# Performance work log

Measured on AMD Instinct MI355X. Metric: run time of the kernel, lower is better.

## Reference

```python
import jax, jax.numpy as jnp
import numpy as np

V, E, H, LM, LC = 50257, 512, 1024, 128, 256


def gru_cell(x, h, Wih, Whh, bih, bhh):
    # PyTorch nn.GRU cell, gate order (r, z, n)
    gi = x @ Wih.T + bih
    gh = h @ Whh.T + bhh
    i_r, i_z, i_n = jnp.split(gi, 3, -1)
    h_r, h_z, h_n = jnp.split(gh, 3, -1)
    r = jax.nn.sigmoid(i_r + h_r)
    z = jax.nn.sigmoid(i_z + h_z)
    n = jnp.tanh(i_n + r * h_n)
    return (1.0 - z) * n + z * h


def setup_inputs() -> dict:
    key = jax.random.key(0)
    ks = jax.random.split(key, 18)
    f = lambda k, sh: jax.random.normal(k, sh, jnp.float32) * 0.02
    return {
        "motion": jax.random.randint(ks[0], (1, LM), 0, V),
        "target_output": jax.random.randint(ks[1], (1, LC), 0, V),
        "enc_emb": f(ks[2], (V, E)),
        "enc_Wih": f(ks[3], (3 * H, E)),
        "enc_Whh": f(ks[4], (3 * H, H)),
        "enc_bih": f(ks[5], (3 * H,)),
        "enc_bhh": f(ks[6], (3 * H,)),
        "dec_emb": f(ks[7], (V, H)),
        "dec_Wih": f(ks[8], (3 * H, H)),
        "dec_Whh": f(ks[9], (3 * H, H)),
        "dec_bih": f(ks[10], (3 * H,)),
        "dec_bhh": f(ks[11], (3 * H,)),
        "attn_W": f(ks[12], (LM, 2 * H)),
        "attn_b": f(ks[13], (LM,)),
        "comb_W": f(ks[14], (H, 2 * H)),
        "comb_b": f(ks[15], (H,)),
        "out_W": f(ks[16], (V, H)),
        "out_b": f(ks[17], (V,)),
    }


def reference(motion, target_output, enc_emb, enc_Wih, enc_Whh, enc_bih, enc_bhh,
              dec_emb, dec_Wih, dec_Whh, dec_bih, dec_bhh,
              attn_W, attn_b, comb_W, comb_b, out_W, out_b):
    # ----- encode: per-step GRU over motion tokens (batch is hard-coded 1) -----
    toks = motion[0]  # [LM]

    def enc_step(h, t):
        h2 = gru_cell(enc_emb[t], h, enc_Wih, enc_Whh, enc_bih, enc_bhh)
        return h2, h2

    h0 = jnp.zeros((H,), jnp.float32)
    enc_h, enc_outs = jax.lax.scan(enc_step, h0, toks)  # enc_outs: [LM, H]

    # ----- decode with teacher forcing -----
    # original: decoder_input = SOS at idx 0, then target[idx-1] set at end of
    # step idx => step idx+1 consumes target[idx-1]; step 1 consumes target[-1].
    tgt = target_output[0]  # [LC]
    dec_in = jnp.concatenate([jnp.zeros((1,), tgt.dtype), tgt[-1:], tgt[:-2]])  # [LC]

    def dec_step(h, t):
        emb = dec_emb[t]  # [H] (dropout is identity at inference)
        attn_w = jax.nn.softmax(jnp.concatenate([emb, h]) @ attn_W.T + attn_b)  # [LM]
        ctx = attn_w @ enc_outs  # [H]
        x = jnp.concatenate([emb, ctx]) @ comb_W.T + comb_b  # [H] (no relu in source)
        h2 = gru_cell(x, h, dec_Wih, dec_Whh, dec_bih, dec_bhh)
        logp = jax.nn.log_softmax(h2 @ out_W.T + out_b)  # [V]
        return h2, logp

    _, logps = jax.lax.scan(dec_step, enc_h, dec_in)  # [LC, V]
    return logps[None]  # [1, LC, V] (permute(1,0,2) with batch=1)
```

## Files before the change

### kernel.cpp

```cpp
#include <hip/hip_runtime.h>

#define V_ 50257
#define E_ 512
#define H_ 1024
#define LM_ 128
#define LC_ 256
#define NBLK 256
#define ROWS 12

typedef __attribute__((ext_vector_type(8))) short short8;
typedef __attribute__((ext_vector_type(4))) float f32x4;
typedef unsigned long long u64;

__device__ __forceinline__ unsigned short f2bf(float x) {
  union { float f; unsigned u; } v; v.f = x;
  unsigned r = v.u + 0x7fffu + ((v.u >> 16) & 1u);
  return (unsigned short)(r >> 16);
}
__device__ __forceinline__ float bflo(unsigned u) { union { unsigned u; float f; } v; v.u = u << 16; return v.f; }
__device__ __forceinline__ float bfhi(unsigned u) { union { unsigned u; float f; } v; v.u = u & 0xffff0000u; return v.f; }

__device__ __forceinline__ int grow4(int s, int i0) {
  return (s < 4) ? (i0 + s) : (s < 8) ? (1024 + i0 + (s - 4)) : (2048 + i0 + (s - 8));
}

__device__ __forceinline__ void st_u32(unsigned* p, unsigned v) {
  __hip_atomic_store(p, v, __ATOMIC_RELAXED, __HIP_MEMORY_SCOPE_AGENT);
}
__device__ __forceinline__ void st_u64(u64* p, u64 v) {
  __hip_atomic_store(p, v, __ATOMIC_RELAXED, __HIP_MEMORY_SCOPE_AGENT);
}
__device__ __forceinline__ u64 ld_u64(const u64* p) {
  return __hip_atomic_load(p, __ATOMIC_RELAXED, __HIP_MEMORY_SCOPE_AGENT);
}
__device__ __forceinline__ unsigned ld_u32(const unsigned* p) {
  return __hip_atomic_load(p, __ATOMIC_RELAXED, __HIP_MEMORY_SCOPE_AGENT);
}
__device__ __forceinline__ float ld_f32(const float* p) {
  return __hip_atomic_load(p, __ATOMIC_RELAXED, __HIP_MEMORY_SCOPE_AGENT);
}
__device__ __forceinline__ void atom_add_f32(float* p, float v) {
  (void)__hip_atomic_fetch_add(p, v, __ATOMIC_RELAXED, __HIP_MEMORY_SCOPE_AGENT);
}

__device__ __forceinline__ void wait_flags4(const unsigned* flags, unsigned need, int tid) {
  if (tid < 64) {
    for (;;) {
      unsigned f0 = ld_u32(&flags[tid * 16]);
      unsigned f1 = ld_u32(&flags[(tid + 64) * 16]);
      unsigned f2 = ld_u32(&flags[(tid + 128) * 16]);
      unsigned f3 = ld_u32(&flags[(tid + 192) * 16]);
      unsigned mn = min(min(f0, f1), min(f2, f3));
      if (__all((int)(mn >= need))) break;
      __builtin_amdgcn_s_sleep(2);
    }
  }
  __syncthreads();
}

__global__ void gather_enc(const int* __restrict__ motion, const float* __restrict__ emb,
                           float* __restrict__ dst) {
  int t = blockIdx.x;
  int tok = motion[t];
  const float4* s = (const float4*)(emb + (size_t)tok * E_);
  float4* d = (float4*)(dst + (size_t)t * E_);
  d[threadIdx.x] = s[threadIdx.x];
}

__global__ void gather_dec(const int* __restrict__ tgt, const float* __restrict__ emb,
                           float* __restrict__ dst) {
  int t = blockIdx.x;
  int tok = (t == 0) ? 0 : (t == 1 ? tgt[LC_ - 1] : tgt[t - 2]);
  const float4* s = (const float4*)(emb + (size_t)tok * H_);
  float4* d = (float4*)(dst + (size_t)t * H_);
  d[threadIdx.x] = s[threadIdx.x];
}

__global__ __launch_bounds__(256) void gemm_f32(const float* __restrict__ A, int lda,
                                                const float* __restrict__ B, int ldb,
                                                const float* __restrict__ bias,
                                                float* __restrict__ C, int ldc, int K) {
  __shared__ float As[16][68];
  __shared__ float Bs[16][68];
  const int bm = blockIdx.y * 64, bn = blockIdx.x * 64;
  const int tid = threadIdx.x;
  const int tx = tid & 15, ty = tid >> 4;
  const int lm = tid & 63, lk = (tid >> 6) * 4;
  float acc[4][4] = {};
  for (int k0 = 0; k0 < K; k0 += 16) {
    float4 av = *(const float4*)&A[(size_t)(bm + lm) * lda + k0 + lk];
    float4 bv = *(const float4*)&B[(size_t)(bn + lm) * ldb + k0 + lk];
    As[lk + 0][lm] = av.x; As[lk + 1][lm] = av.y; As[lk + 2][lm] = av.z; As[lk + 3][lm] = av.w;
    Bs[lk + 0][lm] = bv.x; Bs[lk + 1][lm] = bv.y; Bs[lk + 2][lm] = bv.z; Bs[lk + 3][lm] = bv.w;
    __syncthreads();
#pragma unroll
    for (int kk = 0; kk < 16; ++kk) {
      float4 a4 = *(const float4*)&As[kk][ty * 4];
      float4 b4 = *(const float4*)&Bs[kk][tx * 4];
      acc[0][0] += a4.x * b4.x; acc[0][1] += a4.x * b4.y; acc[0][2] += a4.x * b4.z; acc[0][3] += a4.x * b4.w;
      acc[1][0] += a4.y * b4.x; acc[1][1] += a4.y * b4.y; acc[1][2] += a4.y * b4.z; acc[1][3] += a4.y * b4.w;
      acc[2][0] += a4.z * b4.x; acc[2][1] += a4.z * b4.y; acc[2][2] += a4.z * b4.z; acc[2][3] += a4.z * b4.w;
      acc[3][0] += a4.w * b4.x; acc[3][1] += a4.w * b4.y; acc[3][2] += a4.w * b4.z; acc[3][3] += a4.w * b4.w;
    }
    __syncthreads();
  }
#pragma unroll
  for (int i = 0; i < 4; ++i) {
#pragma unroll
    for (int j = 0; j < 4; ++j) {
      int gm = bm + ty * 4 + i, gn = bn + tx * 4 + j;
      float bv = bias ? bias[gn] : 0.f;
      C[(size_t)gm * ldc + gn] = acc[i][j] + bv;
    }
  }
}

__global__ __launch_bounds__(256) void enc_rnn(const float* __restrict__ Whh,
                                               const float* __restrict__ bhh,
                                               const float* __restrict__ gi,
                                               u64* __restrict__ hx,
                                               unsigned* __restrict__ eflags,
                                               float* __restrict__ outs) {
  __shared__ unsigned short Whl[ROWS][1024];
  __shared__ unsigned h_sh[512];
  __shared__ float h_own[4];
  __shared__ float bh[ROWS];
  __shared__ float ghl[ROWS];
  const int b = blockIdx.x, tid = threadIdx.x;
  const int w = tid >> 6, l = tid & 63;
  const int i0 = b * 4;
  for (int idx = tid; idx < ROWS * 1024; idx += 256) {
    int s = idx >> 10, c = idx & 1023;
    Whl[s][c] = f2bf(Whh[(size_t)grow4(s, i0) * H_ + c]);
  }
  if (tid < ROWS) bh[tid] = bhh[grow4(tid, i0)];
  if (tid < 4) h_own[tid] = 0.f;
  __syncthreads();

  for (int t = 0; t < LM_; ++t) {
    if (t == 0) {
      h_sh[2 * tid] = 0u; h_sh[2 * tid + 1] = 0u;
    } else {
      wait_flags4(eflags, (unsigned)t, tid);
      u64 v = ld_u64(&hx[(t & 1) * 256 + tid]);
      h_sh[2 * tid] = (unsigned)v;
      h_sh[2 * tid + 1] = (unsigned)(v >> 32);
    }
    __syncthreads();

    for (int s = w; s < ROWS; s += 4) {
      float acc = 0.f;
#pragma unroll
      for (int e = 0; e < 8; ++e) {
        unsigned u = *(const unsigned*)&Whl[s][2 * (e * 64 + l)];
        unsigned hv = h_sh[e * 64 + l];
        acc += bflo(u) * bflo(hv) + bfhi(u) * bfhi(hv);
      }
#pragma unroll
      for (int off = 32; off; off >>= 1) acc += __shfl_xor(acc, off);
      if (l == 0) ghl[s] = acc;
    }
    __syncthreads();
    float hpv = 0.f;
    if (tid < 4) {
      int i = tid, ig = i0 + i;
      const float* git = gi + (size_t)t * 3072;
      float gr = git[ig], gz = git[1024 + ig], gn = git[2048 + ig];
      float hr = ghl[i] + bh[i], hz = ghl[4 + i] + bh[4 + i], hn = ghl[8 + i] + bh[8 + i];
      float r = 1.f / (1.f + expf(-(gr + hr)));
      float z = 1.f / (1.f + expf(-(gz + hz)));
      float n = tanhf(gn + r * hn);
      hpv = (1.f - z) * n + z * h_own[i];
      h_own[i] = hpv;
      outs[(size_t)t * H_ + ig] = hpv;
      float v0 = __shfl(hpv, 0), v1 = __shfl(hpv, 1);
      float v2 = __shfl(hpv, 2), v3 = __shfl(hpv, 3);
      if (tid == 0) {
        u64 pk = (u64)((unsigned)f2bf(v0) | ((unsigned)f2bf(v1) << 16))
               | ((u64)((unsigned)f2bf(v2) | ((unsigned)f2bf(v3) << 16)) << 32);
        st_u64(&hx[((t + 1) & 1) * 256 + b], pk);
      }
    }
    __syncthreads();
    if (tid == 0) st_u32(&eflags[b * 16], (unsigned)(t + 1));
  }
}

__global__ __launch_bounds__(256) void dec_rnn(const float* __restrict__ Whh,
                                               const float* __restrict__ bhh,
                                               const float* __restrict__ attn_W,
                                               const float* __restrict__ G,
                                               const float* __restrict__ P1,
                                               const float* __restrict__ aE,
                                               const float* __restrict__ hfin,
                                               float* __restrict__ a_acc,
                                               u64* __restrict__ hx,
                                               unsigned* __restrict__ dflags,
                                               unsigned short* __restrict__ Hs) {
  __shared__ unsigned short Whl[ROWS][1024];
  __shared__ unsigned Ac[2 * 128];
  __shared__ float Gl[ROWS][128];
  __shared__ unsigned h_sh[512];
  __shared__ float a_f[128];
  __shared__ float h_own[4];
  __shared__ float bh[ROWS];
  __shared__ float ghl[ROWS];
  __shared__ float giS[ROWS];
  const int b = blockIdx.x, tid = threadIdx.x;
  const int w = tid >> 6, l = tid & 63;
  const int i0 = b * 4;
  for (int idx = tid; idx < ROWS * 1024; idx += 256) {
    int s = idx >> 10, c = idx & 1023;
    Whl[s][c] = f2bf(Whh[(size_t)grow4(s, i0) * H_ + c]);
  }
  if (tid < 256) {
    int u = tid >> 7, j = tid & 127;
    float2 wv = *(const float2*)&attn_W[(size_t)j * 2048 + 1024 + i0 + 2 * u];
    Ac[tid] = (unsigned)f2bf(wv.x) | ((unsigned)f2bf(wv.y) << 16);
  }
  for (int idx = tid; idx < ROWS * 128; idx += 256) {
    int s = idx >> 7, c = idx & 127;
    Gl[s][c] = G[(size_t)grow4(s, i0) * 128 + c];
  }
  if (tid < ROWS) bh[tid] = bhh[grow4(tid, i0)];
  if (tid < 4) h_own[tid] = hfin[i0 + tid];
  __syncthreads();

  {
    float h0 = h_own[0], h1 = h_own[1], h2 = h_own[2], h3 = h_own[3];
    if (tid < 128) {
      unsigned w0 = Ac[tid], w1 = Ac[128 + tid];
      float a0 = bflo(w0) * h0 + bfhi(w0) * h1 + bflo(w1) * h2 + bfhi(w1) * h3;
      atom_add_f32(&a_acc[(b & 3) * 128 + tid], a0);
    }
    __syncthreads();
    if (tid == 0) st_u32(&dflags[b * 16], 1u);
  }

  for (int t = 0; t < LC_; ++t) {
    wait_flags4(dflags, (unsigned)(t + 1), tid);
    if (t == 0) {
      float4 hv = ((const float4*)hfin)[tid];
      h_sh[2 * tid] = (unsigned)f2bf(hv.x) | ((unsigned)f2bf(hv.y) << 16);
      h_sh[2 * tid + 1] = (unsigned)f2bf(hv.z) | ((unsigned)f2bf(hv.w) << 16);
    } else {
      u64 v = ld_u64(&hx[(t & 1) * 256 + tid]);
      h_sh[2 * tid] = (unsigned)v;
      h_sh[2 * tid + 1] = (unsigned)(v >> 32);
    }
    if (tid < 128) {
      const float* ab = a_acc + (size_t)t * 512;
      a_f[tid] = ld_f32(&ab[tid]) + ld_f32(&ab[128 + tid]) + ld_f32(&ab[256 + tid])
               + ld_f32(&ab[384 + tid]) + aE[(size_t)t * LM_ + tid];
    }
    __syncthreads();

    float ax = a_f[2 * l], ay = a_f[2 * l + 1];
    float mx = fmaxf(ax, ay);
#pragma unroll
    for (int off = 32; off; off >>= 1) mx = fmaxf(mx, __shfl_xor(mx, off));
    float pe0 = expf(ax - mx), pe1 = expf(ay - mx);
    float zs = pe0 + pe1;
#pragma unroll
    for (int off = 32; off; off >>= 1) zs += __shfl_xor(zs, off);
    float w0 = pe0 / zs, w1 = pe1 / zs;
    for (int s = w; s < ROWS; s += 4) {
      float2 g2 = *(const float2*)&Gl[s][2 * l];
      float acc = g2.x * w0 + g2.y * w1;
#pragma unroll
      for (int off = 32; off; off >>= 1) acc += __shfl_xor(acc, off);
      if (l == 0) giS[s] = acc + P1[(size_t)t * 3072 + grow4(s, i0)];
    }
    for (int s = w; s < ROWS; s += 4) {
      float acc = 0.f;
#pragma unroll
      for (int e = 0; e < 8; ++e) {
        unsigned u = *(const unsigned*)&Whl[s][2 * (e * 64 + l)];
        unsigned hv = h_sh[e * 64 + l];
        acc += bflo(u) * bflo(hv) + bfhi(u) * bfhi(hv);
      }
#pragma unroll
      for (int off = 32; off; off >>= 1) acc += __shfl_xor(acc, off);
      if (l == 0) ghl[s] = acc;
    }
    __syncthreads();

    float hpv = 0.f;
    if (tid < 4) {
      int i = tid, ig = i0 + i;
      float hr = ghl[i] + bh[i], hz = ghl[4 + i] + bh[4 + i], hn = ghl[8 + i] + bh[8 + i];
      float r = 1.f / (1.f + expf(-(giS[i] + hr)));
      float z = 1.f / (1.f + expf(-(giS[4 + i] + hz)));
      float n = tanhf(giS[8 + i] + r * hn);
      hpv = (1.f - z) * n + z * h_own[i];
      h_own[i] = hpv;
      Hs[(size_t)t * H_ + ig] = f2bf(hpv);
      if (t < LC_ - 1) {
        float v0 = __shfl(hpv, 0), v1 = __shfl(hpv, 1);
        float v2 = __shfl(hpv, 2), v3 = __shfl(hpv, 3);
        if (tid == 0) {
          u64 pk = (u64)((unsigned)f2bf(v0) | ((unsigned)f2bf(v1) << 16))
                 | ((u64)((unsigned)f2bf(v2) | ((unsigned)f2bf(v3) << 16)) << 32);
          st_u64(&hx[((t + 1) & 1) * 256 + b], pk);
        }
      }
    }
    __syncthreads();
    if (t < LC_ - 1) {
      float h0 = h_own[0], h1 = h_own[1], h2 = h_own[2], h3 = h_own[3];
      if (tid < 128) {
        unsigned w0p = Ac[tid], w1p = Ac[128 + tid];
        float a0 = bflo(w0p) * h0 + bfhi(w0p) * h1 + bflo(w1p) * h2 + bfhi(w1p) * h3;
        atom_add_f32(&a_acc[(size_t)(t + 1) * 512 + (b & 3) * 128 + tid], a0);
      }
    }
    __syncthreads();
    if (tid == 0) st_u32(&dflags[b * 16], (unsigned)(t + 2));
  }
}

__global__ __launch_bounds__(256) void out_gemm(const unsigned short* __restrict__ A,
                                                const float* __restrict__ Wf,
                                                const float* __restrict__ bias,
                                                float* __restrict__ C, int N, int K) {
  __shared__ unsigned short As[256][40];
  __shared__ unsigned short Bs[64][40];
  const int bn = blockIdx.x * 64;
  const int tid = threadIdx.x, w = tid >> 6, l = tid & 63;
  f32x4 acc[4][4];
#pragma unroll
  for (int mf = 0; mf < 4; ++mf)
#pragma unroll
    for (int nf = 0; nf < 4; ++nf) acc[mf][nf] = (f32x4){0.f, 0.f, 0.f, 0.f};

  for (int k0 = 0; k0 < K; k0 += 32) {
    const unsigned short* src = A + (size_t)tid * K + k0;
#pragma unroll
    for (int kc = 0; kc < 4; ++kc) {
      short8 v = *(const short8*)(src + kc * 8);
      *(short8*)&As[tid][kc * 8] = v;
    }
#pragma unroll
    for (int c = 0; c < 2; ++c) {
      int idx = tid + c * 256;
      int n = idx >> 3, kc = idx & 7;
      int gn = bn + n;
      float4 v = {0.f, 0.f, 0.f, 0.f};
      if (gn < N) v = *(const float4*)&Wf[(size_t)gn * K + k0 + kc * 4];
      uint2 p;
      p.x = (unsigned)f2bf(v.x) | ((unsigned)f2bf(v.y) << 16);
      p.y = (unsigned)f2bf(v.z) | ((unsigned)f2bf(v.w) << 16);
      *(uint2*)&Bs[n][kc * 4] = p;
    }
    __syncthreads();
    const int k8 = (l >> 4) * 8;
    short8 af4[4], bf4[4];
#pragma unroll
    for (int mf = 0; mf < 4; ++mf) af4[mf] = *(const short8*)&As[w * 64 + mf * 16 + (l & 15)][k8];
#pragma unroll
    for (int nf = 0; nf < 4; ++nf) bf4[nf] = *(const short8*)&Bs[nf * 16 + (l & 15)][k8];
#pragma unroll
    for (int mf = 0; mf < 4; ++mf)
#pragma unroll
      for (int nf = 0; nf < 4; ++nf)
        acc[mf][nf] = __builtin_amdgcn_mfma_f32_16x16x32_bf16(af4[mf], bf4[nf], acc[mf][nf], 0, 0, 0);
    __syncthreads();
  }
#pragma unroll
  for (int mf = 0; mf < 4; ++mf) {
#pragma unroll
    for (int nf = 0; nf < 4; ++nf) {
      int n = bn + nf * 16 + (l & 15);
      if (n < N) {
        float bv = bias[n];
#pragma unroll
        for (int i = 0; i < 4; ++i) {
          int m = w * 64 + mf * 16 + (l >> 4) * 4 + i;
          C[(size_t)m * N + n] = acc[mf][nf][i] + bv;
        }
      }
    }
  }
}

__global__ __launch_bounds__(256) void lsm_stats(const float* __restrict__ C, float* __restrict__ stats, int N) {
  const int r = blockIdx.x, tid = threadIdx.x, w = tid >> 6, l = tid & 63;
  __shared__ float red[4];
  const float* row = C + (size_t)r * N;
  float m = -3.4e38f;
  for (int i = tid; i < N; i += 256) m = fmaxf(m, row[i]);
#pragma unroll
  for (int off = 32; off; off >>= 1) m = fmaxf(m, __shfl_xor(m, off));
  if (l == 0) red[w] = m;
  __syncthreads();
  m = fmaxf(fmaxf(red[0], red[1]), fmaxf(red[2], red[3]));
  __syncthreads();
  float s = 0.f;
  for (int i = tid; i < N; i += 256) s += expf(row[i] - m);
#pragma unroll
  for (int off = 32; off; off >>= 1) s += __shfl_xor(s, off);
  if (l == 0) red[w] = s;
  __syncthreads();
  if (tid == 0) {
    stats[r] = m;
    stats[256 + r] = logf(red[0] + red[1] + red[2] + red[3]);
  }
}

__global__ __launch_bounds__(256) void lsm_apply(float* __restrict__ C, const float* __restrict__ stats, int N) {
  int r = blockIdx.y;
  int ci = blockIdx.x * 256 + threadIdx.x;
  if (ci < N) {
    size_t idx = (size_t)r * N + ci;
    C[idx] = C[idx] - stats[r] - stats[256 + r];
  }
}

extern "C" void kernel_launch(void* const* d_in, const int* in_sizes, int n_in,
                              void* d_out, int out_size, void* d_ws, size_t ws_size,
                              hipStream_t stream) {
  (void)in_sizes; (void)n_in; (void)out_size; (void)ws_size;
  const int* motion = (const int*)d_in[0];
  const int* tgt = (const int*)d_in[1];
  const float* enc_emb = (const float*)d_in[2];
  const float* enc_Wih = (const float*)d_in[3];
  const float* enc_Whh = (const float*)d_in[4];
  const float* enc_bih = (const float*)d_in[5];
  const float* enc_bhh = (const float*)d_in[6];
  const float* dec_emb = (const float*)d_in[7];
  const float* dec_Wih = (const float*)d_in[8];
  const float* dec_Whh = (const float*)d_in[9];
  const float* dec_bih = (const float*)d_in[10];
  const float* dec_bhh = (const float*)d_in[11];
  const float* attn_W = (const float*)d_in[12];
  const float* attn_b = (const float*)d_in[13];
  const float* comb_W = (const float*)d_in[14];
  const float* comb_b = (const float*)d_in[15];
  const float* out_W = (const float*)d_in[16];
  const float* out_b = (const float*)d_in[17];
  float* out = (float*)d_out;

  float* wsf = (float*)d_ws;
  size_t o = 0;
  auto F = [&](size_t n) { float* p = wsf + o; o += (n + 3) & ~(size_t)3; return p; };
  float* enc_gi = F(128 * 3072);
  float* enc_outs = F(128 * 1024);
  float* embA = F(128 * 512);
  float* demb = F(256 * 1024);
  float* aE = F(256 * 128);
  float* xE = F(256 * 1024);
  float* P1 = F(256 * 3072);
  float* M2T = F(128 * 1024);
  float* Gm = F(3072 * 128);
  u64* hx = (u64*)F(1024);
  unsigned* eflags = (unsigned*)F(4096);
  unsigned* dflags = (unsigned*)F(4096);
  float* a_acc = F(LC_ * 4 * 128);
  float* stats = F(512);
  unsigned short* Hs = (unsigned short*)F(256 * 1024 / 2);

  hipMemsetAsync(eflags, 0, (4096 + 4096 + LC_ * 4 * 128) * sizeof(float), stream);

  gather_enc<<<128, 128, 0, stream>>>(motion, enc_emb, embA);
  gemm_f32<<<dim3(48, 2), 256, 0, stream>>>(embA, 512, enc_Wih, 512, enc_bih, enc_gi, 3072, 512);
  gather_dec<<<256, 256, 0, stream>>>(tgt, dec_emb, demb);
  gemm_f32<<<dim3(2, 4), 256, 0, stream>>>(demb, 1024, attn_W, 2048, attn_b, aE, 128, 1024);
  gemm_f32<<<dim3(16, 4), 256, 0, stream>>>(demb, 1024, comb_W, 2048, comb_b, xE, 1024, 1024);
  gemm_f32<<<dim3(48, 4), 256, 0, stream>>>(xE, 1024, dec_Wih, 1024, dec_bih, P1, 3072, 1024);

  enc_rnn<<<NBLK, 256, 0, stream>>>(enc_Whh, enc_bhh, enc_gi, hx, eflags, enc_outs);

  gemm_f32<<<dim3(16, 2), 256, 0, stream>>>(enc_outs, 1024, comb_W + 1024, 2048, nullptr, M2T, 1024, 1024);
  gemm_f32<<<dim3(2, 48), 256, 0, stream>>>(dec_Wih, 1024, M2T, 1024, nullptr, Gm, 128, 1024);

  dec_rnn<<<NBLK, 256, 0, stream>>>(dec_Whh, dec_bhh, attn_W, Gm, P1, aE,
                                    enc_outs + (size_t)(LM_ - 1) * H_, a_acc, hx, dflags, Hs);

  out_gemm<<<786, 256, 0, stream>>>(Hs, out_W, out_b, out, V_, 1024);
  lsm_stats<<<256, 256, 0, stream>>>(out, stats, V_);
  lsm_apply<<<dim3(197, 256), 256, 0, stream>>>(out, stats, V_);
}
```

Measured before the change: 2.701 ms.

## Tag hidden-state packets with step counters and overlap recurrent matvec with flag wait

Result: slower. 2.845 ms (+5.3%).

```diff
diff --git a/kernel.cpp b/kernel.cpp
--- a/kernel.cpp
+++ b/kernel.cpp
@@ -43,21 +43,6 @@
   (void)__hip_atomic_fetch_add(p, v, __ATOMIC_RELAXED, __HIP_MEMORY_SCOPE_AGENT);
 }
 
-__device__ __forceinline__ void wait_flags4(const unsigned* flags, unsigned need, int tid) {
-  if (tid < 64) {
-    for (;;) {
-      unsigned f0 = ld_u32(&flags[tid * 16]);
-      unsigned f1 = ld_u32(&flags[(tid + 64) * 16]);
-      unsigned f2 = ld_u32(&flags[(tid + 128) * 16]);
-      unsigned f3 = ld_u32(&flags[(tid + 192) * 16]);
-      unsigned mn = min(min(f0, f1), min(f2, f3));
-      if (__all((int)(mn >= need))) break;
-      __builtin_amdgcn_s_sleep(2);
-    }
-  }
-  __syncthreads();
-}
-
 __global__ void gather_enc(const int* __restrict__ motion, const float* __restrict__ emb,
                            float* __restrict__ dst) {
   int t = blockIdx.x;
@@ -74,6 +59,16 @@
   const float4* s = (const float4*)(emb + (size_t)tok * H_);
   float4* d = (float4*)(dst + (size_t)t * H_);
   d[threadIdx.x] = s[threadIdx.x];
+}
+
+__global__ void cvt_bf16(const float* __restrict__ src, u64* __restrict__ dst, int n) {
+  int i = (blockIdx.x * 256 + threadIdx.x) * 4;
+  if (i < n) {
+    float4 v = *(const float4*)&src[i];
+    u64 pk = (u64)((unsigned)f2bf(v.x) | ((unsigned)f2bf(v.y) << 16))
+           | ((u64)((unsigned)f2bf(v.z) | ((unsigned)f2bf(v.w) << 16)) << 32);
+    dst[i >> 2] = pk;
+  }
 }
 
 __global__ __launch_bounds__(256) void gemm_f32(const float* __restrict__ A, int lda,
@@ -118,8 +113,7 @@
 __global__ __launch_bounds__(256) void enc_rnn(const float* __restrict__ Whh,
                                                const float* __restrict__ bhh,
                                                const float* __restrict__ gi,
-                                               u64* __restrict__ hx,
-                                               unsigned* __restrict__ eflags,
+                                               u64* __restrict__ epk,
                                                float* __restrict__ outs) {
   __shared__ unsigned short Whl[ROWS][1024];
   __shared__ unsigned h_sh[512];
@@ -141,10 +135,15 @@
     if (t == 0) {
       h_sh[2 * tid] = 0u; h_sh[2 * tid + 1] = 0u;
     } else {
-      wait_flags4(eflags, (unsigned)t, tid);
-      u64 v = ld_u64(&hx[(t & 1) * 256 + tid]);
-      h_sh[2 * tid] = (unsigned)v;
-      h_sh[2 * tid + 1] = (unsigned)(v >> 32);
+      const u64* pb = epk + (size_t)(t & 1) * 512 + 2 * tid;
+      const unsigned g = (unsigned)t;
+      u64 q0, q1;
+      for (;;) {
+        q0 = ld_u64(pb); q1 = ld_u64(pb + 1);
+        if ((unsigned)(q0 >> 32) == g && (unsigned)(q1 >> 32) == g) break;
+      }
+      h_sh[2 * tid] = (unsigned)q0;
+      h_sh[2 * tid + 1] = (unsigned)q1;
     }
     __syncthreads();
 
@@ -161,7 +160,6 @@
       if (l == 0) ghl[s] = acc;
     }
     __syncthreads();
-    float hpv = 0.f;
     if (tid < 4) {
       int i = tid, ig = i0 + i;
       const float* git = gi + (size_t)t * 3072;
@@ -170,19 +168,18 @@
       float r = 1.f / (1.f + expf(-(gr + hr)));
       float z = 1.f / (1.f + expf(-(gz + hz)));
       float n = tanhf(gn + r * hn);
-      hpv = (1.f - z) * n + z * h_own[i];
+      float hpv = (1.f - z) * n + z * h_own[i];
       h_own[i] = hpv;
       outs[(size_t)t * H_ + ig] = hpv;
       float v0 = __shfl(hpv, 0), v1 = __shfl(hpv, 1);
       float v2 = __shfl(hpv, 2), v3 = __shfl(hpv, 3);
       if (tid == 0) {
-        u64 pk = (u64)((unsigned)f2bf(v0) | ((unsigned)f2bf(v1) << 16))
-               | ((u64)((unsigned)f2bf(v2) | ((unsigned)f2bf(v3) << 16)) << 32);
-        st_u64(&hx[((t + 1) & 1) * 256 + b], pk);
-      }
-    }
-    __syncthreads();
-    if (tid == 0) st_u32(&eflags[b * 16], (unsigned)(t + 1));
+        u64 gg = (u64)(unsigned)(t + 1) << 32;
+        u64* pb = epk + (size_t)((t + 1) & 1) * 512 + 2 * b;
+        st_u64(pb,     gg | (u64)((unsigned)f2bf(v0) | ((unsigned)f2bf(v1) << 16)));
+        st_u64(pb + 1, gg | (u64)((unsigned)f2bf(v2) | ((unsigned)f2bf(v3) << 16)));
+      }
+    }
   }
 }
 
@@ -194,7 +191,7 @@
                                                const float* __restrict__ aE,
                                                const float* __restrict__ hfin,
                                                float* __restrict__ a_acc,
-                                               u64* __restrict__ hx,
+                                               u64* __restrict__ dpk,
                                                unsigned* __restrict__ dflags,
                                                unsigned short* __restrict__ Hs) {
   __shared__ unsigned short Whl[ROWS][1024];
@@ -238,20 +235,52 @@
   }
 
   for (int t = 0; t < LC_; ++t) {
-    wait_flags4(dflags, (unsigned)(t + 1), tid);
     if (t == 0) {
       float4 hv = ((const float4*)hfin)[tid];
       h_sh[2 * tid] = (unsigned)f2bf(hv.x) | ((unsigned)f2bf(hv.y) << 16);
       h_sh[2 * tid + 1] = (unsigned)f2bf(hv.z) | ((unsigned)f2bf(hv.w) << 16);
     } else {
-      u64 v = ld_u64(&hx[(t & 1) * 256 + tid]);
-      h_sh[2 * tid] = (unsigned)v;
-      h_sh[2 * tid + 1] = (unsigned)(v >> 32);
-    }
-    if (tid < 128) {
+      const u64* pb = dpk + (size_t)(t & 1) * 512 + 2 * tid;
+      const unsigned g = (unsigned)t;
+      u64 q0, q1;
+      for (;;) {
+        q0 = ld_u64(pb); q1 = ld_u64(pb + 1);
+        if ((unsigned)(q0 >> 32) == g && (unsigned)(q1 >> 32) == g) break;
+      }
+      h_sh[2 * tid] = (unsigned)q0;
+      h_sh[2 * tid + 1] = (unsigned)q1;
+    }
+    __syncthreads();
+
+    for (int s = w; s < ROWS; s += 4) {
+      float acc = 0.f;
+#pragma unroll
+      for (int e = 0; e < 8; ++e) {
+        unsigned u = *(const unsigned*)&Whl[s][2 * (e * 64 + l)];
+        unsigned hv = h_sh[e * 64 + l];
+        acc += bflo(u) * bflo(hv) + bfhi(u) * bfhi(hv);
+      }
+#pragma unroll
+      for (int off = 32; off; off >>= 1) acc += __shfl_xor(acc, off);
+      if (l == 0) ghl[s] = acc;
+    }
+    if (tid < 64) {
+      const unsigned need = (unsigned)(t + 1);
+      for (;;) {
+        unsigned f0 = ld_u32(&dflags[tid * 16]);
+        unsigned f1 = ld_u32(&dflags[(tid + 64) * 16]);
+        unsigned f2 = ld_u32(&dflags[(tid + 128) * 16]);
+        unsigned f3 = ld_u32(&dflags[(tid + 192) * 16]);
+        unsigned mn = min(min(f0, f1), min(f2, f3));
+        if (__all((int)(mn >= need))) break;
+      }
       const float* ab = a_acc + (size_t)t * 512;
-      a_f[tid] = ld_f32(&ab[tid]) + ld_f32(&ab[128 + tid]) + ld_f32(&ab[256 + tid])
-               + ld_f32(&ab[384 + tid]) + aE[(size_t)t * LM_ + tid];
+      float s0 = ld_f32(&ab[2 * l]) + ld_f32(&ab[128 + 2 * l])
+               + ld_f32(&ab[256 + 2 * l]) + ld_f32(&ab[384 + 2 * l]);
+      float s1 = ld_f32(&ab[2 * l + 1]) + ld_f32(&ab[128 + 2 * l + 1])
+               + ld_f32(&ab[256 + 2 * l + 1]) + ld_f32(&ab[384 + 2 * l + 1]);
+      a_f[2 * l] = s0 + aE[(size_t)t * LM_ + 2 * l];
+      a_f[2 * l + 1] = s1 + aE[(size_t)t * LM_ + 2 * l + 1];
     }
     __syncthreads();
 
@@ -271,41 +300,30 @@
       for (int off = 32; off; off >>= 1) acc += __shfl_xor(acc, off);
       if (l == 0) giS[s] = acc + P1[(size_t)t * 3072 + grow4(s, i0)];
     }
-    for (int s = w; s < ROWS; s += 4) {
-      float acc = 0.f;
-#pragma unroll
-      for (int e = 0; e < 8; ++e) {
-        unsigned u = *(const unsigned*)&Whl[s][2 * (e * 64 + l)];
-        unsigned hv = h_sh[e * 64 + l];
-        acc += bflo(u) * bflo(hv) + bfhi(u) * bfhi(hv);
-      }
-#pragma unroll
-      for (int off = 32; off; off >>= 1) acc += __shfl_xor(acc, off);
-      if (l == 0) ghl[s] = acc;
-    }
-    __syncthreads();
-
-    float hpv = 0.f;
+    __syncthreads();
+
     if (tid < 4) {
       int i = tid, ig = i0 + i;
       float hr = ghl[i] + bh[i], hz = ghl[4 + i] + bh[4 + i], hn = ghl[8 + i] + bh[8 + i];
       float r = 1.f / (1.f + expf(-(giS[i] + hr)));
       float z = 1.f / (1.f + expf(-(giS[4 + i] + hz)));
       float n = tanhf(giS[8 + i] + r * hn);
-      hpv = (1.f - z) * n + z * h_own[i];
+      float hpv = (1.f - z) * n + z * h_own[i];
       h_own[i] = hpv;
       Hs[(size_t)t * H_ + ig] = f2bf(hpv);
       if (t < LC_ - 1) {
         float v0 = __shfl(hpv, 0), v1 = __shfl(hpv, 1);
         float v2 = __shfl(hpv, 2), v3 = __shfl(hpv, 3);
         if (tid == 0) {
-          u64 pk = (u64)((unsigned)f2bf(v0) | ((unsigned)f2bf(v1) << 16))
-                 | ((u64)((unsigned)f2bf(v2) | ((unsigned)f2bf(v3) << 16)) << 32);
-          st_u64(&hx[((t + 1) & 1) * 256 + b], pk);
+          u64 gg = (u64)(unsigned)(t + 1) << 32;
+          u64* pb = dpk + (size_t)((t + 1) & 1) * 512 + 2 * b;
+          st_u64(pb,     gg | (u64)((unsigned)f2bf(v0) | ((unsigned)f2bf(v1) << 16)));
+          st_u64(pb + 1, gg | (u64)((unsigned)f2bf(v2) | ((unsigned)f2bf(v3) << 16)));
         }
       }
     }
     __syncthreads();
+
     if (t < LC_ - 1) {
       float h0 = h_own[0], h1 = h_own[1], h2 = h_own[2], h3 = h_own[3];
       if (tid < 128) {
@@ -320,7 +338,7 @@
 }
 
 __global__ __launch_bounds__(256) void out_gemm(const unsigned short* __restrict__ A,
-                                                const float* __restrict__ Wf,
+                                                const float* __restrict__ Wf, int ldw,
                                                 const float* __restrict__ bias,
                                                 float* __restrict__ C, int N, int K) {
   __shared__ unsigned short As[256][40];
@@ -346,7 +364,7 @@
       int n = idx >> 3, kc = idx & 7;
       int gn = bn + n;
       float4 v = {0.f, 0.f, 0.f, 0.f};
-      if (gn < N) v = *(const float4*)&Wf[(size_t)gn * K + k0 + kc * 4];
+      if (gn < N) v = *(const float4*)&Wf[(size_t)gn * ldw + k0 + kc * 4];
       uint2 p;
       p.x = (unsigned)f2bf(v.x) | ((unsigned)f2bf(v.y) << 16);
       p.y = (unsigned)f2bf(v.z) | ((unsigned)f2bf(v.w) << 16);
@@ -452,31 +470,35 @@
   float* P1 = F(256 * 3072);
   float* M2T = F(128 * 1024);
   float* Gm = F(3072 * 128);
-  u64* hx = (u64*)F(1024);
-  unsigned* eflags = (unsigned*)F(4096);
+  unsigned short* demb_bf = (unsigned short*)F(131072);
+  unsigned short* xE_bf = (unsigned short*)F(131072);
+  u64* epk = (u64*)F(2048);
+  u64* dpk = (u64*)F(2048);
   unsigned* dflags = (unsigned*)F(4096);
-  float* a_acc = F(LC_ * 4 * 128);
+  float* a_acc = F(LC_ * 512);
   float* stats = F(512);
   unsigned short* Hs = (unsigned short*)F(256 * 1024 / 2);
 
-  hipMemsetAsync(eflags, 0, (4096 + 4096 + LC_ * 4 * 128) * sizeof(float), stream);
+  hipMemsetAsync(epk, 0, (2048 + 2048 + 4096 + LC_ * 512) * sizeof(float), stream);
 
   gather_enc<<<128, 128, 0, stream>>>(motion, enc_emb, embA);
   gemm_f32<<<dim3(48, 2), 256, 0, stream>>>(embA, 512, enc_Wih, 512, enc_bih, enc_gi, 3072, 512);
   gather_dec<<<256, 256, 0, stream>>>(tgt, dec_emb, demb);
-  gemm_f32<<<dim3(2, 4), 256, 0, stream>>>(demb, 1024, attn_W, 2048, attn_b, aE, 128, 1024);
-  gemm_f32<<<dim3(16, 4), 256, 0, stream>>>(demb, 1024, comb_W, 2048, comb_b, xE, 1024, 1024);
-  gemm_f32<<<dim3(48, 4), 256, 0, stream>>>(xE, 1024, dec_Wih, 1024, dec_bih, P1, 3072, 1024);
-
-  enc_rnn<<<NBLK, 256, 0, stream>>>(enc_Whh, enc_bhh, enc_gi, hx, eflags, enc_outs);
+  cvt_bf16<<<256, 256, 0, stream>>>(demb, (u64*)demb_bf, 256 * 1024);
+  out_gemm<<<2, 256, 0, stream>>>(demb_bf, attn_W, 2048, attn_b, aE, 128, 1024);
+  out_gemm<<<16, 256, 0, stream>>>(demb_bf, comb_W, 2048, comb_b, xE, 1024, 1024);
+  cvt_bf16<<<256, 256, 0, stream>>>(xE, (u64*)xE_bf, 256 * 1024);
+  out_gemm<<<48, 256, 0, stream>>>(xE_bf, dec_Wih, 1024, dec_bih, P1, 3072, 1024);
+
+  enc_rnn<<<NBLK, 256, 0, stream>>>(enc_Whh, enc_bhh, enc_gi, epk, enc_outs);
 
   gemm_f32<<<dim3(16, 2), 256, 0, stream>>>(enc_outs, 1024, comb_W + 1024, 2048, nullptr, M2T, 1024, 1024);
   gemm_f32<<<dim3(2, 48), 256, 0, stream>>>(dec_Wih, 1024, M2T, 1024, nullptr, Gm, 128, 1024);
 
   dec_rnn<<<NBLK, 256, 0, stream>>>(dec_Whh, dec_bhh, attn_W, Gm, P1, aE,
-                                    enc_outs + (size_t)(LM_ - 1) * H_, a_acc, hx, dflags, Hs);
-
-  out_gemm<<<786, 256, 0, stream>>>(Hs, out_W, out_b, out, V_, 1024);
+                                    enc_outs + (size_t)(LM_ - 1) * H_, a_acc, dpk, dflags, Hs);
+
+  out_gemm<<<786, 256, 0, stream>>>(Hs, out_W, 1024, out_b, out, V_, 1024);
   lsm_stats<<<256, 256, 0, stream>>>(out, stats, V_);
   lsm_apply<<<dim3(197, 256), 256, 0, stream>>>(out, stats, V_);
 }
```
